# Kernel tuning notes

Hardware: AMD Instinct MI355X
Metric: run time of the kernel (lower is better)

## Reference

```python
import jax, jax.numpy as jnp
import numpy as np

N_NODES = 100000
N_EDGES = 1600000
F_IN = 128
F_OUT = 32


def setup_inputs() -> dict:
    key = jax.random.key(0)
    k1, k2, k3 = jax.random.split(key, 3)
    x = jax.random.normal(k1, (N_NODES, F_IN), dtype=jnp.float32)
    edge_index = jax.random.randint(k2, (2, N_EDGES), 0, N_NODES, dtype=jnp.int64)
    # Glorot-style init for the GCNConv linear weight [F_IN, F_OUT]
    W = jax.random.normal(k3, (F_IN, F_OUT), dtype=jnp.float32) * (1.0 / np.sqrt(F_IN))
    b = jnp.zeros((F_OUT,), dtype=jnp.float32)
    return {"x": x, "edge_index": edge_index, "W": W, "b": b}


def reference(x, edge_index, W, b):
    N = x.shape[0]
    # --- add self loops (PyG GCNConv default) ---
    loops = jnp.arange(N, dtype=edge_index.dtype)
    src = jnp.concatenate([edge_index[0], loops])  # message sources j
    dst = jnp.concatenate([edge_index[1], loops])  # aggregation targets i
    # --- symmetric normalization: deg^-1/2[src] * deg^-1/2[dst] ---
    ones = jnp.ones(src.shape[0], dtype=x.dtype)
    deg = jax.ops.segment_sum(ones, dst, num_segments=N)  # in-degree incl. self loop
    dinv = jnp.where(deg > 0, jax.lax.rsqrt(deg), jnp.zeros_like(deg))
    norm = dinv[src] * dinv[dst]  # [E+N]
    # --- linear transform then gather-scale-scatter aggregate ---
    h = x @ W  # [N, F_OUT]
    msgs = h[src] * norm[:, None]  # [E+N, F_OUT]
    out = jax.ops.segment_sum(msgs, dst, num_segments=N)  # [N, F_OUT]
    return out + b
```

## Files before the change

kernel.cpp:

```cpp
#include <hip/hip_runtime.h>
#include <hip/hip_fp16.h>

#define N_NODES 100000
#define N_EDGES 1600000
#define F_IN    128
#define F_OUT   32

#define BKT_SHIFT  7
#define BKT_SIZE   128
#define NBKT       782
#define BKT_STRIDE 2560

#define BIN_THREADS 512
#define BIN_TILE    8192
#define EPT         (BIN_TILE / BIN_THREADS)
#define NTILES      ((N_EDGES + BIN_TILE - 1) / BIN_TILE)

#define AGG_SPLIT  4
#define SUB        32
#define SUB_STRIDE 768

typedef _Float16 f16x8 __attribute__((ext_vector_type(8)));
typedef float    f32x4 __attribute__((ext_vector_type(4)));

__global__ void init_kernel(int* __restrict__ gcur) {
    int i = blockIdx.x * blockDim.x + threadIdx.x;
    if (i < NBKT) gcur[i] = 0;
}

__global__ __launch_bounds__(BIN_THREADS) void bin_kernel(const int* __restrict__ ei,
                                                          int* __restrict__ gcur,
                                                          unsigned int* __restrict__ binned) {
    __shared__ int cnt[NBKT], gbase[NBKT];
    int t = threadIdx.x;
    for (int b = t; b < NBKT; b += BIN_THREADS) cnt[b] = 0;
    __syncthreads();
    int ebase = blockIdx.x * BIN_TILE;
    unsigned int pk[EPT];
    int rk[EPT];
    short bkt[EPT];
#pragma unroll
    for (int k = 0; k < EPT; ++k) {
        int e = ebase + k * BIN_THREADS + t;
        if (e < N_EDGES) {
            int s = ei[e];
            int d = ei[N_EDGES + e];
            bkt[k] = (short)(d >> BKT_SHIFT);
            pk[k]  = (unsigned)s | ((unsigned)(d & (BKT_SIZE - 1)) << 25);
            rk[k]  = atomicAdd(&cnt[bkt[k]], 1);
        } else {
            bkt[k] = -1;
        }
    }
    __syncthreads();
    for (int b = t; b < NBKT; b += BIN_THREADS)
        if (cnt[b] > 0) gbase[b] = atomicAdd(&gcur[b], cnt[b]);
    __syncthreads();
#pragma unroll
    for (int k = 0; k < EPT; ++k) {
        if (bkt[k] >= 0) {
            int p = gbase[bkt[k]] + rk[k];
            if (p < BKT_STRIDE)
                binned[(size_t)bkt[k] * BKT_STRIDE + p] = pk[k];
        }
    }
}

#define WH_STRIDE 136
__global__ __launch_bounds__(512) void matmul_kernel(const float4* __restrict__ x4,
                                                     const float* __restrict__ W,
                                                     const unsigned int* __restrict__ binned,
                                                     const int* __restrict__ gcur,
                                                     __half* __restrict__ hs) {
    __shared__ _Float16 Wh[F_OUT * WH_STRIDE];
    __shared__ int cnt128[BKT_SIZE];
    __shared__ float dinvL[BKT_SIZE];
    int t = threadIdx.x;
    int b = blockIdx.x;

    if (t < BKT_SIZE) cnt128[t] = 0;
    {
        int col = t & 31, kb = (t >> 5) * 8;
        for (int u = 0; u < 8; ++u)
            Wh[col * WH_STRIDE + kb + u] = (_Float16)W[(kb + u) * F_OUT + col];
    }
    __syncthreads();

    int ne = gcur[b];
    if (ne > BKT_STRIDE) ne = BKT_STRIDE;
    const unsigned int* eb = binned + (size_t)b * BKT_STRIDE;
    for (int i = t; i < ne; i += 512)
        atomicAdd(&cnt128[eb[i] >> 25], 1);
    __syncthreads();
    if (t < BKT_SIZE) dinvL[t] = rsqrtf((float)(cnt128[t] + 1));
    __syncthreads();

    int w = t >> 6, l = t & 63;
    int lr = l & 15, kg = l >> 4;
    int row = b * 128 + w * 16 + lr;
    const float4* xr = x4 + (size_t)row * 32;
    bool rok = row < N_NODES;

    f16x8 a[4];
#pragma unroll
    for (int ks = 0; ks < 4; ++ks) {
        float4 v0, v1;
        if (rok) {
            v0 = xr[ks * 8 + kg * 2];
            v1 = xr[ks * 8 + kg * 2 + 1];
        } else {
            v0 = make_float4(0, 0, 0, 0);
            v1 = v0;
        }
        f16x8 av;
        av[0] = (_Float16)v0.x; av[1] = (_Float16)v0.y;
        av[2] = (_Float16)v0.z; av[3] = (_Float16)v0.w;
        av[4] = (_Float16)v1.x; av[5] = (_Float16)v1.y;
        av[6] = (_Float16)v1.z; av[7] = (_Float16)v1.w;
        a[ks] = av;
    }

    f32x4 c0 = {0.f, 0.f, 0.f, 0.f}, c1 = {0.f, 0.f, 0.f, 0.f};
#pragma unroll
    for (int ks = 0; ks < 4; ++ks) {
        f16x8 b0 = *(const f16x8*)&Wh[lr * WH_STRIDE + ks * 32 + kg * 8];
        f16x8 b1 = *(const f16x8*)&Wh[(16 + lr) * WH_STRIDE + ks * 32 + kg * 8];
        c0 = __builtin_amdgcn_mfma_f32_16x16x32_f16(a[ks], b0, c0, 0, 0, 0);
        c1 = __builtin_amdgcn_mfma_f32_16x16x32_f16(a[ks], b1, c1, 0, 0, 0);
    }

    int lrow0 = w * 16 + kg * 4;
#pragma unroll
    for (int i = 0; i < 4; ++i) {
        int orow = b * 128 + lrow0 + i;
        if (orow < N_NODES) {
            float dv = dinvL[lrow0 + i];
            hs[(size_t)orow * F_OUT + lr]      = (__half)(c0[i] * dv);
            hs[(size_t)orow * F_OUT + 16 + lr] = (__half)(c1[i] * dv);
        }
    }
}

__device__ inline void acc4(uint2 u, float& a0, float& a1, float& a2, float& a3) {
    float2 f0 = __half22float2(*(__half2*)&u.x);
    float2 f1 = __half22float2(*(__half2*)&u.y);
    a0 += f0.x; a1 += f0.y; a2 += f1.x; a3 += f1.y;
}

__global__ __launch_bounds__(256) void aggregate_kernel(const unsigned int* __restrict__ binned,
                                                        const int* __restrict__ gcur,
                                                        const uint2* __restrict__ hs4,
                                                        const float* __restrict__ bias,
                                                        float* __restrict__ out) {
    __shared__ int cnt[SUB];
    __shared__ int sc[SUB];
    __shared__ int rp[SUB + 1];
    __shared__ int se[SUB_STRIDE];
    int t = threadIdx.x;
    int b   = blockIdx.x >> 2;
    int sub = blockIdx.x & 3;
    int ne = gcur[b];
    if (ne > BKT_STRIDE) ne = BKT_STRIDE;
    const unsigned int* eb = binned + (size_t)b * BKT_STRIDE;

    if (t < SUB) cnt[t] = 0;
    __syncthreads();

    unsigned pk[10];
    int rk[10];
#pragma unroll
    for (int k = 0; k < 10; ++k) {
        int i = t + k * 256;
        pk[k] = (i < ne) ? eb[i] : 0xFFFFFFFFu;
    }
#pragma unroll
    for (int k = 0; k < 10; ++k) {
        rk[k] = -1;
        if (pk[k] != 0xFFFFFFFFu) {
            int dl = (int)(pk[k] >> 25);
            if ((dl >> 5) == sub) rk[k] = atomicAdd(&cnt[dl & 31], 1);
        }
    }
    __syncthreads();
    int v = (t < SUB) ? cnt[t] : 0;
    if (t < SUB) sc[t] = v;
    __syncthreads();
    for (int off = 1; off < SUB; off <<= 1) {
        int add = (t < SUB && t >= off) ? sc[t - off] : 0;
        __syncthreads();
        if (t < SUB) sc[t] += add;
        __syncthreads();
    }
    if (t < SUB) {
        int ex = sc[t] - v;
        rp[t] = (ex < SUB_STRIDE) ? ex : SUB_STRIDE;
    }
    if (t == 0) rp[SUB] = 0;
    __syncthreads();
    if (t == 0) {
        int tot = sc[SUB - 1];
        rp[SUB] = (tot > SUB_STRIDE) ? SUB_STRIDE : tot;
    }
    __syncthreads();
#pragma unroll
    for (int k = 0; k < 10; ++k) {
        if (rk[k] >= 0) {
            int dl = (int)(pk[k] >> 25);
            int pos = rp[dl & 31] + rk[k];
            if (pos < SUB_STRIDE) se[pos] = (int)(pk[k] & 0x1FFFFFF);
        }
    }
    __syncthreads();

    int n = t >> 3, j4 = t & 7;
    int gnode = b * BKT_SIZE + sub * SUB + n;
    if (gnode >= N_NODES) return;
    float4 bv = *(const float4*)&bias[j4 * 4];
    int deg = cnt[n];
    int beg = rp[n];
    int end = rp[n + 1];
    if (beg + deg < end) end = beg + deg;
    float a0 = 0.f, a1 = 0.f, a2 = 0.f, a3 = 0.f;
    int p = beg;
    for (; p + 7 < end; p += 8) {
        uint2 u0 = hs4[(size_t)se[p]     * 8 + j4];
        uint2 u1 = hs4[(size_t)se[p + 1] * 8 + j4];
        uint2 u2 = hs4[(size_t)se[p + 2] * 8 + j4];
        uint2 u3 = hs4[(size_t)se[p + 3] * 8 + j4];
        uint2 u4 = hs4[(size_t)se[p + 4] * 8 + j4];
        uint2 u5 = hs4[(size_t)se[p + 5] * 8 + j4];
        uint2 u6 = hs4[(size_t)se[p + 6] * 8 + j4];
        uint2 u7 = hs4[(size_t)se[p + 7] * 8 + j4];
        acc4(u0, a0, a1, a2, a3); acc4(u1, a0, a1, a2, a3);
        acc4(u2, a0, a1, a2, a3); acc4(u3, a0, a1, a2, a3);
        acc4(u4, a0, a1, a2, a3); acc4(u5, a0, a1, a2, a3);
        acc4(u6, a0, a1, a2, a3); acc4(u7, a0, a1, a2, a3);
    }
    for (; p + 3 < end; p += 4) {
        uint2 u0 = hs4[(size_t)se[p]     * 8 + j4];
        uint2 u1 = hs4[(size_t)se[p + 1] * 8 + j4];
        uint2 u2 = hs4[(size_t)se[p + 2] * 8 + j4];
        uint2 u3 = hs4[(size_t)se[p + 3] * 8 + j4];
        acc4(u0, a0, a1, a2, a3); acc4(u1, a0, a1, a2, a3);
        acc4(u2, a0, a1, a2, a3); acc4(u3, a0, a1, a2, a3);
    }
    for (; p < end; ++p) {
        uint2 u0 = hs4[(size_t)se[p] * 8 + j4];
        acc4(u0, a0, a1, a2, a3);
    }
    float dv = rsqrtf((float)(deg + 1));
    uint2 us = hs4[(size_t)gnode * 8 + j4];
    float2 s0 = __half22float2(*(__half2*)&us.x);
    float2 s1 = __half22float2(*(__half2*)&us.y);
    float4 o;
    o.x = bv.x + dv * (a0 + s0.x);
    o.y = bv.y + dv * (a1 + s0.y);
    o.z = bv.z + dv * (a2 + s1.x);
    o.w = bv.w + dv * (a3 + s1.y);
    *(float4*)&out[(size_t)gnode * F_OUT + j4 * 4] = o;
}

extern "C" void kernel_launch(void* const* d_in, const int* in_sizes, int n_in,
                              void* d_out, int out_size, void* d_ws, size_t ws_size,
                              hipStream_t stream) {
    const float* x  = (const float*)d_in[0];
    const int*   ei = (const int*)d_in[1];
    const float* W  = (const float*)d_in[2];
    const float* b  = (const float*)d_in[3];
    float* out = (float*)d_out;

    int*          gcur   = (int*)d_ws;
    unsigned int* binned = (unsigned int*)(gcur + 1024);
    __half*       hs     = (__half*)(binned + (size_t)NBKT * BKT_STRIDE);

    init_kernel<<<1, 1024, 0, stream>>>(gcur);

    bin_kernel<<<NTILES, BIN_THREADS, 0, stream>>>(ei, gcur, binned);

    matmul_kernel<<<NBKT, 512, 0, stream>>>((const float4*)x, W, binned, gcur, hs);

    aggregate_kernel<<<NBKT * AGG_SPLIT, 256, 0, stream>>>(binned, gcur, (const uint2*)hs, b, out);
}
```

Baseline: 68.08 us.

## Aggregate whole bucket per block with 16-byte gathers, memset init

The aggregation kernel now handles an entire 128-node bucket per 512-thread block instead of splitting each bucket across four blocks. Each block reads and sorts the bucket's edge list once rather than four times. Each thread now gathers 8 fp16 features per edge with uint4 loads, so four threads cover a node instead of eight. The init kernel is replaced by hipMemsetAsync, and the overflow clamps on sub-bucket positions are removed; this relies on bucket counts never exceeding BKT_STRIDE. In exchange there are fewer, larger blocks and more registers per thread.

```diff
diff --git a/kernel.cpp b/kernel.cpp
--- a/kernel.cpp
+++ b/kernel.cpp
@@ -16,17 +16,8 @@
 #define EPT         (BIN_TILE / BIN_THREADS)
 #define NTILES      ((N_EDGES + BIN_TILE - 1) / BIN_TILE)
 
-#define AGG_SPLIT  4
-#define SUB        32
-#define SUB_STRIDE 768
-
 typedef _Float16 f16x8 __attribute__((ext_vector_type(8)));
 typedef float    f32x4 __attribute__((ext_vector_type(4)));
-
-__global__ void init_kernel(int* __restrict__ gcur) {
-    int i = blockIdx.x * blockDim.x + threadIdx.x;
-    if (i < NBKT) gcur[i] = 0;
-}
 
 __global__ __launch_bounds__(BIN_THREADS) void bin_kernel(const int* __restrict__ ei,
                                                           int* __restrict__ gcur,
@@ -141,123 +132,122 @@
     }
 }
 
-__device__ inline void acc4(uint2 u, float& a0, float& a1, float& a2, float& a3) {
+__device__ inline void acc8(uint4 u, float* a) {
     float2 f0 = __half22float2(*(__half2*)&u.x);
     float2 f1 = __half22float2(*(__half2*)&u.y);
-    a0 += f0.x; a1 += f0.y; a2 += f1.x; a3 += f1.y;
-}
-
-__global__ __launch_bounds__(256) void aggregate_kernel(const unsigned int* __restrict__ binned,
+    float2 f2 = __half22float2(*(__half2*)&u.z);
+    float2 f3 = __half22float2(*(__half2*)&u.w);
+    a[0] += f0.x; a[1] += f0.y; a[2] += f1.x; a[3] += f1.y;
+    a[4] += f2.x; a[5] += f2.y; a[6] += f3.x; a[7] += f3.y;
+}
+
+#define AEPT 5
+__global__ __launch_bounds__(512) void aggregate_kernel(const unsigned int* __restrict__ binned,
                                                         const int* __restrict__ gcur,
-                                                        const uint2* __restrict__ hs4,
+                                                        const uint4* __restrict__ hs8,
                                                         const float* __restrict__ bias,
                                                         float* __restrict__ out) {
-    __shared__ int cnt[SUB];
-    __shared__ int sc[SUB];
-    __shared__ int rp[SUB + 1];
-    __shared__ int se[SUB_STRIDE];
+    __shared__ int cnt[BKT_SIZE];
+    __shared__ int sc[BKT_SIZE];
+    __shared__ int rp[BKT_SIZE + 1];
+    __shared__ int se[BKT_STRIDE];
     int t = threadIdx.x;
-    int b   = blockIdx.x >> 2;
-    int sub = blockIdx.x & 3;
+    int b = blockIdx.x;
     int ne = gcur[b];
     if (ne > BKT_STRIDE) ne = BKT_STRIDE;
     const unsigned int* eb = binned + (size_t)b * BKT_STRIDE;
 
-    if (t < SUB) cnt[t] = 0;
-    __syncthreads();
-
-    unsigned pk[10];
-    int rk[10];
-#pragma unroll
-    for (int k = 0; k < 10; ++k) {
-        int i = t + k * 256;
+    if (t < BKT_SIZE) cnt[t] = 0;
+    __syncthreads();
+
+    unsigned pk[AEPT];
+    int rk[AEPT];
+#pragma unroll
+    for (int k = 0; k < AEPT; ++k) {
+        int i = t + k * 512;
         pk[k] = (i < ne) ? eb[i] : 0xFFFFFFFFu;
     }
 #pragma unroll
-    for (int k = 0; k < 10; ++k) {
+    for (int k = 0; k < AEPT; ++k) {
         rk[k] = -1;
-        if (pk[k] != 0xFFFFFFFFu) {
-            int dl = (int)(pk[k] >> 25);
-            if ((dl >> 5) == sub) rk[k] = atomicAdd(&cnt[dl & 31], 1);
-        }
-    }
-    __syncthreads();
-    int v = (t < SUB) ? cnt[t] : 0;
-    if (t < SUB) sc[t] = v;
-    __syncthreads();
-    for (int off = 1; off < SUB; off <<= 1) {
-        int add = (t < SUB && t >= off) ? sc[t - off] : 0;
+        if (pk[k] != 0xFFFFFFFFu)
+            rk[k] = atomicAdd(&cnt[pk[k] >> 25], 1);
+    }
+    __syncthreads();
+    int v = (t < BKT_SIZE) ? cnt[t] : 0;
+    if (t < BKT_SIZE) sc[t] = v;
+    __syncthreads();
+    for (int off = 1; off < BKT_SIZE; off <<= 1) {
+        int add = (t < BKT_SIZE && t >= off) ? sc[t - off] : 0;
         __syncthreads();
-        if (t < SUB) sc[t] += add;
+        if (t < BKT_SIZE) sc[t] += add;
         __syncthreads();
     }
-    if (t < SUB) {
-        int ex = sc[t] - v;
-        rp[t] = (ex < SUB_STRIDE) ? ex : SUB_STRIDE;
-    }
-    if (t == 0) rp[SUB] = 0;
-    __syncthreads();
-    if (t == 0) {
-        int tot = sc[SUB - 1];
-        rp[SUB] = (tot > SUB_STRIDE) ? SUB_STRIDE : tot;
-    }
-    __syncthreads();
-#pragma unroll
-    for (int k = 0; k < 10; ++k) {
+    if (t < BKT_SIZE) rp[t] = sc[t] - v;
+    if (t == 0) rp[BKT_SIZE] = ne;
+    __syncthreads();
+#pragma unroll
+    for (int k = 0; k < AEPT; ++k) {
         if (rk[k] >= 0) {
-            int dl = (int)(pk[k] >> 25);
-            int pos = rp[dl & 31] + rk[k];
-            if (pos < SUB_STRIDE) se[pos] = (int)(pk[k] & 0x1FFFFFF);
-        }
-    }
-    __syncthreads();
-
-    int n = t >> 3, j4 = t & 7;
-    int gnode = b * BKT_SIZE + sub * SUB + n;
+            int pos = rp[pk[k] >> 25] + rk[k];
+            se[pos] = (int)(pk[k] & 0x1FFFFFF);
+        }
+    }
+    __syncthreads();
+
+    int n = t >> 2, q = t & 3;
+    int gnode = b * BKT_SIZE + n;
     if (gnode >= N_NODES) return;
-    float4 bv = *(const float4*)&bias[j4 * 4];
-    int deg = cnt[n];
-    int beg = rp[n];
-    int end = rp[n + 1];
-    if (beg + deg < end) end = beg + deg;
-    float a0 = 0.f, a1 = 0.f, a2 = 0.f, a3 = 0.f;
+    int beg = rp[n], end = rp[n + 1];
+    int deg = end - beg;
+    float acc[8] = {0.f, 0.f, 0.f, 0.f, 0.f, 0.f, 0.f, 0.f};
     int p = beg;
     for (; p + 7 < end; p += 8) {
-        uint2 u0 = hs4[(size_t)se[p]     * 8 + j4];
-        uint2 u1 = hs4[(size_t)se[p + 1] * 8 + j4];
-        uint2 u2 = hs4[(size_t)se[p + 2] * 8 + j4];
-        uint2 u3 = hs4[(size_t)se[p + 3] * 8 + j4];
-        uint2 u4 = hs4[(size_t)se[p + 4] * 8 + j4];
-        uint2 u5 = hs4[(size_t)se[p + 5] * 8 + j4];
-        uint2 u6 = hs4[(size_t)se[p + 6] * 8 + j4];
-        uint2 u7 = hs4[(size_t)se[p + 7] * 8 + j4];
-        acc4(u0, a0, a1, a2, a3); acc4(u1, a0, a1, a2, a3);
-        acc4(u2, a0, a1, a2, a3); acc4(u3, a0, a1, a2, a3);
-        acc4(u4, a0, a1, a2, a3); acc4(u5, a0, a1, a2, a3);
-        acc4(u6, a0, a1, a2, a3); acc4(u7, a0, a1, a2, a3);
+        uint4 u0 = hs8[(size_t)se[p]     * 4 + q];
+        uint4 u1 = hs8[(size_t)se[p + 1] * 4 + q];
+        uint4 u2 = hs8[(size_t)se[p + 2] * 4 + q];
+        uint4 u3 = hs8[(size_t)se[p + 3] * 4 + q];
+        uint4 u4 = hs8[(size_t)se[p + 4] * 4 + q];
+        uint4 u5 = hs8[(size_t)se[p + 5] * 4 + q];
+        uint4 u6 = hs8[(size_t)se[p + 6] * 4 + q];
+        uint4 u7 = hs8[(size_t)se[p + 7] * 4 + q];
+        acc8(u0, acc); acc8(u1, acc); acc8(u2, acc); acc8(u3, acc);
+        acc8(u4, acc); acc8(u5, acc); acc8(u6, acc); acc8(u7, acc);
     }
     for (; p + 3 < end; p += 4) {
-        uint2 u0 = hs4[(size_t)se[p]     * 8 + j4];
-        uint2 u1 = hs4[(size_t)se[p + 1] * 8 + j4];
-        uint2 u2 = hs4[(size_t)se[p + 2] * 8 + j4];
-        uint2 u3 = hs4[(size_t)se[p + 3] * 8 + j4];
-        acc4(u0, a0, a1, a2, a3); acc4(u1, a0, a1, a2, a3);
-        acc4(u2, a0, a1, a2, a3); acc4(u3, a0, a1, a2, a3);
-    }
-    for (; p < end; ++p) {
-        uint2 u0 = hs4[(size_t)se[p] * 8 + j4];
-        acc4(u0, a0, a1, a2, a3);
-    }
+        uint4 u0 = hs8[(size_t)se[p]     * 4 + q];
+        uint4 u1 = hs8[(size_t)se[p + 1] * 4 + q];
+        uint4 u2 = hs8[(size_t)se[p + 2] * 4 + q];
+        uint4 u3 = hs8[(size_t)se[p + 3] * 4 + q];
+        acc8(u0, acc); acc8(u1, acc); acc8(u2, acc); acc8(u3, acc);
+    }
+    for (; p < end; ++p)
+        acc8(hs8[(size_t)se[p] * 4 + q], acc);
+
     float dv = rsqrtf((float)(deg + 1));
-    uint2 us = hs4[(size_t)gnode * 8 + j4];
-    float2 s0 = __half22float2(*(__half2*)&us.x);
-    float2 s1 = __half22float2(*(__half2*)&us.y);
-    float4 o;
-    o.x = bv.x + dv * (a0 + s0.x);
-    o.y = bv.y + dv * (a1 + s0.y);
-    o.z = bv.z + dv * (a2 + s1.x);
-    o.w = bv.w + dv * (a3 + s1.y);
-    *(float4*)&out[(size_t)gnode * F_OUT + j4 * 4] = o;
+    uint4 us = hs8[(size_t)gnode * 4 + q];
+    float selfv[8];
+    {
+        float2 f0 = __half22float2(*(__half2*)&us.x);
+        float2 f1 = __half22float2(*(__half2*)&us.y);
+        float2 f2 = __half22float2(*(__half2*)&us.z);
+        float2 f3 = __half22float2(*(__half2*)&us.w);
+        selfv[0] = f0.x; selfv[1] = f0.y; selfv[2] = f1.x; selfv[3] = f1.y;
+        selfv[4] = f2.x; selfv[5] = f2.y; selfv[6] = f3.x; selfv[7] = f3.y;
+    }
+    float4 bv0 = *(const float4*)&bias[q * 8];
+    float4 bv1 = *(const float4*)&bias[q * 8 + 4];
+    float4 o0, o1;
+    o0.x = bv0.x + dv * (acc[0] + selfv[0]);
+    o0.y = bv0.y + dv * (acc[1] + selfv[1]);
+    o0.z = bv0.z + dv * (acc[2] + selfv[2]);
+    o0.w = bv0.w + dv * (acc[3] + selfv[3]);
+    o1.x = bv1.x + dv * (acc[4] + selfv[4]);
+    o1.y = bv1.y + dv * (acc[5] + selfv[5]);
+    o1.z = bv1.z + dv * (acc[6] + selfv[6]);
+    o1.w = bv1.w + dv * (acc[7] + selfv[7]);
+    *(float4*)&out[(size_t)gnode * F_OUT + q * 8]     = o0;
+    *(float4*)&out[(size_t)gnode * F_OUT + q * 8 + 4] = o1;
 }
 
 extern "C" void kernel_launch(void* const* d_in, const int* in_sizes, int n_in,
@@ -273,11 +263,11 @@
     unsigned int* binned = (unsigned int*)(gcur + 1024);
     __half*       hs     = (__half*)(binned + (size_t)NBKT * BKT_STRIDE);
 
-    init_kernel<<<1, 1024, 0, stream>>>(gcur);
+    hipMemsetAsync(gcur, 0, NBKT * sizeof(int), stream);
 
     bin_kernel<<<NTILES, BIN_THREADS, 0, stream>>>(ei, gcur, binned);
 
     matmul_kernel<<<NBKT, 512, 0, stream>>>((const float4*)x, W, binned, gcur, hs);
 
-    aggregate_kernel<<<NBKT * AGG_SPLIT, 256, 0, stream>>>(binned, gcur, (const uint2*)hs, b, out);
-}
+    aggregate_kernel<<<NBKT, 512, 0, stream>>>(binned, gcur, (const uint4*)hs, b, out);
+}
```

After: 70.82 us. +4.0%, slower.

## Run binning and matmul in one launch and apply source normalization during aggregation

Applied to the files above, without the earlier changes.

The binning and the x@W matmul now run as two disjoint block ranges of one kernel, so the matmul no longer waits on the binned degree counts. The source-side deg^-1/2 scaling moves from the matmul epilogue into the aggregation loop, which gathers a per-source dinv value produced by a new small kernel. The init kernel becomes a memset. This adds one launch and an extra random gather of dinv per edge in aggregation, in exchange for overlapping the matmul with binning.

```diff
diff --git a/kernel.cpp b/kernel.cpp
--- a/kernel.cpp
+++ b/kernel.cpp
@@ -23,133 +23,137 @@
 typedef _Float16 f16x8 __attribute__((ext_vector_type(8)));
 typedef float    f32x4 __attribute__((ext_vector_type(4)));
 
-__global__ void init_kernel(int* __restrict__ gcur) {
-    int i = blockIdx.x * blockDim.x + threadIdx.x;
-    if (i < NBKT) gcur[i] = 0;
-}
-
-__global__ __launch_bounds__(BIN_THREADS) void bin_kernel(const int* __restrict__ ei,
-                                                          int* __restrict__ gcur,
-                                                          unsigned int* __restrict__ binned) {
-    __shared__ int cnt[NBKT], gbase[NBKT];
+#define WH_STRIDE 136
+
+__global__ __launch_bounds__(512) void fused_bin_matmul_kernel(const int* __restrict__ ei,
+                                                               int* __restrict__ gcur,
+                                                               unsigned int* __restrict__ binned,
+                                                               const float4* __restrict__ x4,
+                                                               const float* __restrict__ W,
+                                                               __half* __restrict__ hs) {
+    __shared__ char pool[9216];
     int t = threadIdx.x;
-    for (int b = t; b < NBKT; b += BIN_THREADS) cnt[b] = 0;
-    __syncthreads();
-    int ebase = blockIdx.x * BIN_TILE;
-    unsigned int pk[EPT];
-    int rk[EPT];
-    short bkt[EPT];
-#pragma unroll
-    for (int k = 0; k < EPT; ++k) {
-        int e = ebase + k * BIN_THREADS + t;
-        if (e < N_EDGES) {
-            int s = ei[e];
-            int d = ei[N_EDGES + e];
-            bkt[k] = (short)(d >> BKT_SHIFT);
-            pk[k]  = (unsigned)s | ((unsigned)(d & (BKT_SIZE - 1)) << 25);
-            rk[k]  = atomicAdd(&cnt[bkt[k]], 1);
-        } else {
-            bkt[k] = -1;
-        }
-    }
-    __syncthreads();
-    for (int b = t; b < NBKT; b += BIN_THREADS)
-        if (cnt[b] > 0) gbase[b] = atomicAdd(&gcur[b], cnt[b]);
-    __syncthreads();
-#pragma unroll
-    for (int k = 0; k < EPT; ++k) {
-        if (bkt[k] >= 0) {
-            int p = gbase[bkt[k]] + rk[k];
-            if (p < BKT_STRIDE)
-                binned[(size_t)bkt[k] * BKT_STRIDE + p] = pk[k];
-        }
-    }
-}
-
-#define WH_STRIDE 136
-__global__ __launch_bounds__(512) void matmul_kernel(const float4* __restrict__ x4,
-                                                     const float* __restrict__ W,
-                                                     const unsigned int* __restrict__ binned,
-                                                     const int* __restrict__ gcur,
-                                                     __half* __restrict__ hs) {
-    __shared__ _Float16 Wh[F_OUT * WH_STRIDE];
-    __shared__ int cnt128[BKT_SIZE];
-    __shared__ float dinvL[BKT_SIZE];
+
+    if (blockIdx.x < NTILES) {
+        int* cnt   = (int*)pool;
+        int* gbase = cnt + NBKT;
+        for (int b = t; b < NBKT; b += BIN_THREADS) cnt[b] = 0;
+        __syncthreads();
+        int ebase = blockIdx.x * BIN_TILE;
+        unsigned int pk[EPT];
+        int rk[EPT];
+        short bkt[EPT];
+#pragma unroll
+        for (int k = 0; k < EPT; ++k) {
+            int e = ebase + k * BIN_THREADS + t;
+            if (e < N_EDGES) {
+                int s = ei[e];
+                int d = ei[N_EDGES + e];
+                bkt[k] = (short)(d >> BKT_SHIFT);
+                pk[k]  = (unsigned)s | ((unsigned)(d & (BKT_SIZE - 1)) << 25);
+                rk[k]  = atomicAdd(&cnt[bkt[k]], 1);
+            } else {
+                bkt[k] = -1;
+            }
+        }
+        __syncthreads();
+        for (int b = t; b < NBKT; b += BIN_THREADS)
+            if (cnt[b] > 0) gbase[b] = atomicAdd(&gcur[b], cnt[b]);
+        __syncthreads();
+#pragma unroll
+        for (int k = 0; k < EPT; ++k) {
+            if (bkt[k] >= 0) {
+                int p = gbase[bkt[k]] + rk[k];
+                if (p < BKT_STRIDE)
+                    binned[(size_t)bkt[k] * BKT_STRIDE + p] = pk[k];
+            }
+        }
+    } else {
+        _Float16* Wh = (_Float16*)pool;
+        int b = blockIdx.x - NTILES;
+        {
+            int col = t & 31, kb = (t >> 5) * 8;
+            for (int u = 0; u < 8; ++u)
+                Wh[col * WH_STRIDE + kb + u] = (_Float16)W[(kb + u) * F_OUT + col];
+        }
+        __syncthreads();
+
+        int w = t >> 6, l = t & 63;
+        int lr = l & 15, kg = l >> 4;
+        int row = b * 128 + w * 16 + lr;
+        const float4* xr = x4 + (size_t)row * 32;
+        bool rok = row < N_NODES;
+
+        f16x8 a[4];
+#pragma unroll
+        for (int ks = 0; ks < 4; ++ks) {
+            float4 v0, v1;
+            if (rok) {
+                v0 = xr[ks * 8 + kg * 2];
+                v1 = xr[ks * 8 + kg * 2 + 1];
+            } else {
+                v0 = make_float4(0, 0, 0, 0);
+                v1 = v0;
+            }
+            f16x8 av;
+            av[0] = (_Float16)v0.x; av[1] = (_Float16)v0.y;
+            av[2] = (_Float16)v0.z; av[3] = (_Float16)v0.w;
+            av[4] = (_Float16)v1.x; av[5] = (_Float16)v1.y;
+            av[6] = (_Float16)v1.z; av[7] = (_Float16)v1.w;
+            a[ks] = av;
+        }
+
+        f32x4 c0 = {0.f, 0.f, 0.f, 0.f}, c1 = {0.f, 0.f, 0.f, 0.f};
+#pragma unroll
+        for (int ks = 0; ks < 4; ++ks) {
+            f16x8 b0 = *(const f16x8*)&Wh[lr * WH_STRIDE + ks * 32 + kg * 8];
+            f16x8 b1 = *(const f16x8*)&Wh[(16 + lr) * WH_STRIDE + ks * 32 + kg * 8];
+            c0 = __builtin_amdgcn_mfma_f32_16x16x32_f16(a[ks], b0, c0, 0, 0, 0);
+            c1 = __builtin_amdgcn_mfma_f32_16x16x32_f16(a[ks], b1, c1, 0, 0, 0);
+        }
+
+        int lrow0 = w * 16 + kg * 4;
+#pragma unroll
+        for (int i = 0; i < 4; ++i) {
+            int orow = b * 128 + lrow0 + i;
+            if (orow < N_NODES) {
+                hs[(size_t)orow * F_OUT + lr]      = (__half)c0[i];
+                hs[(size_t)orow * F_OUT + 16 + lr] = (__half)c1[i];
+            }
+        }
+    }
+}
+
+__global__ __launch_bounds__(256) void dinv_from_bins_kernel(const unsigned int* __restrict__ binned,
+                                                             const int* __restrict__ gcur,
+                                                             float* __restrict__ dinv) {
+    __shared__ int cnt[BKT_SIZE];
     int t = threadIdx.x;
     int b = blockIdx.x;
-
-    if (t < BKT_SIZE) cnt128[t] = 0;
-    {
-        int col = t & 31, kb = (t >> 5) * 8;
-        for (int u = 0; u < 8; ++u)
-            Wh[col * WH_STRIDE + kb + u] = (_Float16)W[(kb + u) * F_OUT + col];
-    }
-    __syncthreads();
-
+    if (t < BKT_SIZE) cnt[t] = 0;
+    __syncthreads();
     int ne = gcur[b];
     if (ne > BKT_STRIDE) ne = BKT_STRIDE;
     const unsigned int* eb = binned + (size_t)b * BKT_STRIDE;
-    for (int i = t; i < ne; i += 512)
-        atomicAdd(&cnt128[eb[i] >> 25], 1);
-    __syncthreads();
-    if (t < BKT_SIZE) dinvL[t] = rsqrtf((float)(cnt128[t] + 1));
-    __syncthreads();
-
-    int w = t >> 6, l = t & 63;
-    int lr = l & 15, kg = l >> 4;
-    int row = b * 128 + w * 16 + lr;
-    const float4* xr = x4 + (size_t)row * 32;
-    bool rok = row < N_NODES;
-
-    f16x8 a[4];
-#pragma unroll
-    for (int ks = 0; ks < 4; ++ks) {
-        float4 v0, v1;
-        if (rok) {
-            v0 = xr[ks * 8 + kg * 2];
-            v1 = xr[ks * 8 + kg * 2 + 1];
-        } else {
-            v0 = make_float4(0, 0, 0, 0);
-            v1 = v0;
-        }
-        f16x8 av;
-        av[0] = (_Float16)v0.x; av[1] = (_Float16)v0.y;
-        av[2] = (_Float16)v0.z; av[3] = (_Float16)v0.w;
-        av[4] = (_Float16)v1.x; av[5] = (_Float16)v1.y;
-        av[6] = (_Float16)v1.z; av[7] = (_Float16)v1.w;
-        a[ks] = av;
-    }
-
-    f32x4 c0 = {0.f, 0.f, 0.f, 0.f}, c1 = {0.f, 0.f, 0.f, 0.f};
-#pragma unroll
-    for (int ks = 0; ks < 4; ++ks) {
-        f16x8 b0 = *(const f16x8*)&Wh[lr * WH_STRIDE + ks * 32 + kg * 8];
-        f16x8 b1 = *(const f16x8*)&Wh[(16 + lr) * WH_STRIDE + ks * 32 + kg * 8];
-        c0 = __builtin_amdgcn_mfma_f32_16x16x32_f16(a[ks], b0, c0, 0, 0, 0);
-        c1 = __builtin_amdgcn_mfma_f32_16x16x32_f16(a[ks], b1, c1, 0, 0, 0);
-    }
-
-    int lrow0 = w * 16 + kg * 4;
-#pragma unroll
-    for (int i = 0; i < 4; ++i) {
-        int orow = b * 128 + lrow0 + i;
-        if (orow < N_NODES) {
-            float dv = dinvL[lrow0 + i];
-            hs[(size_t)orow * F_OUT + lr]      = (__half)(c0[i] * dv);
-            hs[(size_t)orow * F_OUT + 16 + lr] = (__half)(c1[i] * dv);
-        }
-    }
-}
-
-__device__ inline void acc4(uint2 u, float& a0, float& a1, float& a2, float& a3) {
+    for (int i = t; i < ne; i += 256)
+        atomicAdd(&cnt[eb[i] >> 25], 1);
+    __syncthreads();
+    int gnode = b * BKT_SIZE + t;
+    if (t < BKT_SIZE && gnode < N_NODES)
+        dinv[gnode] = rsqrtf((float)(cnt[t] + 1));
+}
+
+__device__ inline void fma4(uint2 u, float w, float& a0, float& a1, float& a2, float& a3) {
     float2 f0 = __half22float2(*(__half2*)&u.x);
     float2 f1 = __half22float2(*(__half2*)&u.y);
-    a0 += f0.x; a1 += f0.y; a2 += f1.x; a3 += f1.y;
+    a0 = fmaf(f0.x, w, a0); a1 = fmaf(f0.y, w, a1);
+    a2 = fmaf(f1.x, w, a2); a3 = fmaf(f1.y, w, a3);
 }
 
 __global__ __launch_bounds__(256) void aggregate_kernel(const unsigned int* __restrict__ binned,
                                                         const int* __restrict__ gcur,
                                                         const uint2* __restrict__ hs4,
+                                                        const float* __restrict__ dinv,
                                                         const float* __restrict__ bias,
                                                         float* __restrict__ out) {
     __shared__ int cnt[SUB];
@@ -195,8 +199,6 @@
         int ex = sc[t] - v;
         rp[t] = (ex < SUB_STRIDE) ? ex : SUB_STRIDE;
     }
-    if (t == 0) rp[SUB] = 0;
-    __syncthreads();
     if (t == 0) {
         int tot = sc[SUB - 1];
         rp[SUB] = (tot > SUB_STRIDE) ? SUB_STRIDE : tot;
@@ -212,7 +214,8 @@
     }
     __syncthreads();
 
-    int n = t >> 3, j4 = t & 7;
+    int g = t >> 3, j4 = t & 7;
+    int n = g;
     int gnode = b * BKT_SIZE + sub * SUB + n;
     if (gnode >= N_NODES) return;
     float4 bv = *(const float4*)&bias[j4 * 4];
@@ -223,40 +226,44 @@
     float a0 = 0.f, a1 = 0.f, a2 = 0.f, a3 = 0.f;
     int p = beg;
     for (; p + 7 < end; p += 8) {
-        uint2 u0 = hs4[(size_t)se[p]     * 8 + j4];
-        uint2 u1 = hs4[(size_t)se[p + 1] * 8 + j4];
-        uint2 u2 = hs4[(size_t)se[p + 2] * 8 + j4];
-        uint2 u3 = hs4[(size_t)se[p + 3] * 8 + j4];
-        uint2 u4 = hs4[(size_t)se[p + 4] * 8 + j4];
-        uint2 u5 = hs4[(size_t)se[p + 5] * 8 + j4];
-        uint2 u6 = hs4[(size_t)se[p + 6] * 8 + j4];
-        uint2 u7 = hs4[(size_t)se[p + 7] * 8 + j4];
-        acc4(u0, a0, a1, a2, a3); acc4(u1, a0, a1, a2, a3);
-        acc4(u2, a0, a1, a2, a3); acc4(u3, a0, a1, a2, a3);
-        acc4(u4, a0, a1, a2, a3); acc4(u5, a0, a1, a2, a3);
-        acc4(u6, a0, a1, a2, a3); acc4(u7, a0, a1, a2, a3);
+        int s0 = se[p],     s1 = se[p + 1], s2 = se[p + 2], s3 = se[p + 3];
+        int s4 = se[p + 4], s5 = se[p + 5], s6 = se[p + 6], s7 = se[p + 7];
+        uint2 u0 = hs4[(size_t)s0 * 8 + j4]; float w0 = dinv[s0];
+        uint2 u1 = hs4[(size_t)s1 * 8 + j4]; float w1 = dinv[s1];
+        uint2 u2 = hs4[(size_t)s2 * 8 + j4]; float w2 = dinv[s2];
+        uint2 u3 = hs4[(size_t)s3 * 8 + j4]; float w3 = dinv[s3];
+        uint2 u4 = hs4[(size_t)s4 * 8 + j4]; float w4 = dinv[s4];
+        uint2 u5 = hs4[(size_t)s5 * 8 + j4]; float w5 = dinv[s5];
+        uint2 u6 = hs4[(size_t)s6 * 8 + j4]; float w6 = dinv[s6];
+        uint2 u7 = hs4[(size_t)s7 * 8 + j4]; float w7 = dinv[s7];
+        fma4(u0, w0, a0, a1, a2, a3); fma4(u1, w1, a0, a1, a2, a3);
+        fma4(u2, w2, a0, a1, a2, a3); fma4(u3, w3, a0, a1, a2, a3);
+        fma4(u4, w4, a0, a1, a2, a3); fma4(u5, w5, a0, a1, a2, a3);
+        fma4(u6, w6, a0, a1, a2, a3); fma4(u7, w7, a0, a1, a2, a3);
     }
     for (; p + 3 < end; p += 4) {
-        uint2 u0 = hs4[(size_t)se[p]     * 8 + j4];
-        uint2 u1 = hs4[(size_t)se[p + 1] * 8 + j4];
-        uint2 u2 = hs4[(size_t)se[p + 2] * 8 + j4];
-        uint2 u3 = hs4[(size_t)se[p + 3] * 8 + j4];
-        acc4(u0, a0, a1, a2, a3); acc4(u1, a0, a1, a2, a3);
-        acc4(u2, a0, a1, a2, a3); acc4(u3, a0, a1, a2, a3);
+        int s0 = se[p], s1 = se[p + 1], s2 = se[p + 2], s3 = se[p + 3];
+        uint2 u0 = hs4[(size_t)s0 * 8 + j4]; float w0 = dinv[s0];
+        uint2 u1 = hs4[(size_t)s1 * 8 + j4]; float w1 = dinv[s1];
+        uint2 u2 = hs4[(size_t)s2 * 8 + j4]; float w2 = dinv[s2];
+        uint2 u3 = hs4[(size_t)s3 * 8 + j4]; float w3 = dinv[s3];
+        fma4(u0, w0, a0, a1, a2, a3); fma4(u1, w1, a0, a1, a2, a3);
+        fma4(u2, w2, a0, a1, a2, a3); fma4(u3, w3, a0, a1, a2, a3);
     }
     for (; p < end; ++p) {
-        uint2 u0 = hs4[(size_t)se[p] * 8 + j4];
-        acc4(u0, a0, a1, a2, a3);
+        int s0 = se[p];
+        uint2 u0 = hs4[(size_t)s0 * 8 + j4]; float w0 = dinv[s0];
+        fma4(u0, w0, a0, a1, a2, a3);
     }
     float dv = rsqrtf((float)(deg + 1));
     uint2 us = hs4[(size_t)gnode * 8 + j4];
     float2 s0 = __half22float2(*(__half2*)&us.x);
     float2 s1 = __half22float2(*(__half2*)&us.y);
     float4 o;
-    o.x = bv.x + dv * (a0 + s0.x);
-    o.y = bv.y + dv * (a1 + s0.y);
-    o.z = bv.z + dv * (a2 + s1.x);
-    o.w = bv.w + dv * (a3 + s1.y);
+    o.x = bv.x + dv * (a0 + dv * s0.x);
+    o.y = bv.y + dv * (a1 + dv * s0.y);
+    o.z = bv.z + dv * (a2 + dv * s1.x);
+    o.w = bv.w + dv * (a3 + dv * s1.y);
     *(float4*)&out[(size_t)gnode * F_OUT + j4 * 4] = o;
 }
 
@@ -271,13 +278,16 @@
 
     int*          gcur   = (int*)d_ws;
     unsigned int* binned = (unsigned int*)(gcur + 1024);
-    __half*       hs     = (__half*)(binned + (size_t)NBKT * BKT_STRIDE);
-
-    init_kernel<<<1, 1024, 0, stream>>>(gcur);
-
-    bin_kernel<<<NTILES, BIN_THREADS, 0, stream>>>(ei, gcur, binned);
-
-    matmul_kernel<<<NBKT, 512, 0, stream>>>((const float4*)x, W, binned, gcur, hs);
-
-    aggregate_kernel<<<NBKT * AGG_SPLIT, 256, 0, stream>>>(binned, gcur, (const uint2*)hs, b, out);
-}
+    float*        dinv   = (float*)(binned + (size_t)NBKT * BKT_STRIDE);
+    __half*       hs     = (__half*)(dinv + ((N_NODES + 3) & ~3));
+
+    hipMemsetAsync(gcur, 0, NBKT * sizeof(int), stream);
+
+    fused_bin_matmul_kernel<<<NTILES + NBKT, 512, 0, stream>>>(ei, gcur, binned,
+                                                               (const float4*)x, W, hs);
+
+    dinv_from_bins_kernel<<<NBKT, 256, 0, stream>>>(binned, gcur, dinv);
+
+    aggregate_kernel<<<NBKT * AGG_SPLIT, 256, 0, stream>>>(binned, gcur, (const uint2*)hs,
+                                                           dinv, b, out);
+}
```

New measurement: 71.40 us. +4.9%, slower.
